# Performance work log

Measured on AMD Instinct MI355X. Metric: run time of the kernel, lower is better.

## Reference

```python
import jax, jax.numpy as jnp
import numpy as np

N = 10000      # nodes
E = 100000     # edges per direction
DIN = 128      # input feature dim (== hidden so layers stack)
H = 4          # attention heads
C = 128        # out channels per head (concat=False -> mean over heads)
ED = 16        # edge_attr dim
L = 2          # number of layers (len(hidden_sizes))
NEG_SLOPE = 0.2
EPS = 1e-5


def setup_inputs() -> dict:
    key = jax.random.key(0)
    ks = jax.random.split(key, 32)
    f32 = jnp.float32

    def nrm(k, shape, s=0.05):
        return jax.random.normal(k, shape, dtype=f32) * s

    inp = {}
    inp["x"] = nrm(ks[0], (N, DIN), 1.0)
    inp["fwd_edges_index"] = jax.random.randint(ks[1], (2, E), 0, N, dtype=jnp.int32)
    inp["bwd_edges_index"] = jax.random.randint(ks[2], (2, E), 0, N, dtype=jnp.int32)
    inp["edge_attr"] = nrm(ks[3], (E, ED), 1.0)
    # GATv2 params, stacked over layers; suffix _f = FWDGATLayer, _b = BWDGATLayer
    for i, sfx in enumerate(["f", "b"]):
        o = 4 + 7 * i
        inp[f"Wl_{sfx}"] = nrm(ks[o + 0], (L, DIN, H * C))   # lin_l (source x_j)
        inp[f"bl_{sfx}"] = jnp.zeros((L, H * C), f32)
        inp[f"Wr_{sfx}"] = nrm(ks[o + 1], (L, DIN, H * C))   # lin_r (target x_i)
        inp[f"br_{sfx}"] = jnp.zeros((L, H * C), f32)
        inp[f"We_{sfx}"] = nrm(ks[o + 2], (L, ED, H * C))    # lin_edge (no bias)
        inp[f"att_{sfx}"] = nrm(ks[o + 3], (L, H, C))        # attention vector a
        inp[f"bias_{sfx}"] = jnp.zeros((L, C), f32)          # final bias (concat=False)
    # Merge MLP: Linear(2C,C) -> ReLU -> Linear(C,C)
    inp["Wm1"] = nrm(ks[20], (L, 2 * C, C)); inp["bm1"] = jnp.zeros((L, C), f32)
    inp["Wm2"] = nrm(ks[21], (L, C, C));     inp["bm2"] = jnp.zeros((L, C), f32)
    # BatchNorm affine params (training-mode batch stats)
    inp["gamma"] = jnp.ones((L, C), f32)
    inp["beta"] = jnp.zeros((L, C), f32)
    return inp


def gatv2(x, src, dst, eattr, Wl, bl, Wr, br, We, att, bias):
    """PyG GATv2Conv, heads=H, concat=False (mean over heads), share_weights=False."""
    xl = (x @ Wl + bl).reshape(N, H, C)          # source-side transform (x_j)
    xr = (x @ Wr + br).reshape(N, H, C)          # target-side transform (x_i)
    ee = (eattr @ We).reshape(E, H, C)           # edge embedding
    z = jax.nn.leaky_relu(xl[src] + xr[dst] + ee, NEG_SLOPE)   # [E,H,C]
    logits = jnp.einsum('ehc,hc->eh', z, att)    # per-edge per-head scores
    # scatter-softmax over incoming edges of each target node
    amax = jax.lax.stop_gradient(jax.ops.segment_max(logits, dst, num_segments=N))
    amax = jnp.where(jnp.isfinite(amax), amax, 0.0)  # nodes with no in-edges
    ex = jnp.exp(logits - amax[dst])
    denom = jax.ops.segment_sum(ex, dst, num_segments=N)
    alpha = ex / denom[dst]                      # [E,H]
    msg = (xl[src] * alpha[:, :, None]).reshape(E, H * C)
    agg = jax.ops.segment_sum(msg, dst, num_segments=N).reshape(N, H, C)
    return agg.mean(axis=1) + bias               # concat=False -> head mean


def batch_norm(x, gamma, beta):
    mu = x.mean(axis=0)
    var = x.var(axis=0)  # biased var, as torch BN uses for normalization
    return gamma * (x - mu) * jax.lax.rsqrt(var + EPS) + beta


def reference(x, fwd_edges_index, bwd_edges_index, edge_attr,
              Wl_f, bl_f, Wr_f, br_f, We_f, att_f, bias_f,
              Wl_b, bl_b, Wr_b, br_b, We_b, att_b, bias_b,
              Wm1, bm1, Wm2, bm2, gamma, beta):
    fs, fd = fwd_edges_index[0], fwd_edges_index[1]
    bs, bd = bwd_edges_index[0], bwd_edges_index[1]
    h = x
    for l in range(L):
        f = gatv2(h, fs, fd, edge_attr, Wl_f[l], bl_f[l], Wr_f[l], br_f[l],
                  We_f[l], att_f[l], bias_f[l])
        b = gatv2(h, bs, bd, edge_attr, Wl_b[l], bl_b[l], Wr_b[l], br_b[l],
                  We_b[l], att_b[l], bias_b[l])
        m = jnp.concatenate([f, b], axis=1)                     # [N, 2C]
        m = jax.nn.relu(m @ Wm1[l] + bm1[l]) @ Wm2[l] + bm2[l]  # merge MLP
        h = jax.nn.relu(batch_norm(m, gamma[l], beta[l]))
    return h
```

## Files before the change

kernel.cpp:

```cpp
#include <hip/hip_runtime.h>

constexpr int N_  = 10000;
constexpr int E_  = 100000;
constexpr int MP_ = 10112;

typedef unsigned int u32;
typedef unsigned short u16;
typedef __attribute__((ext_vector_type(8))) _Float16 f16x8;
typedef __attribute__((ext_vector_type(4))) _Float16 f16x4;
typedef __attribute__((ext_vector_type(2))) _Float16 f16x2;
typedef __attribute__((ext_vector_type(4))) float f32x4;

__device__ __forceinline__ u16 f2h(float f) {
  _Float16 h = (_Float16)f;
  u16 r;
  __builtin_memcpy(&r, &h, 2);
  return r;
}
__device__ __forceinline__ void async16(const void* g, void* l) {
  __builtin_amdgcn_global_load_lds((const __attribute__((address_space(1))) u32*)g,
                                   (__attribute__((address_space(3))) u32*)l, 16, 0, 0);
}


__global__ void k_prep(const float* __restrict__ Wl_f, const float* __restrict__ Wr_f,
                       const float* __restrict__ Wl_b, const float* __restrict__ Wr_b,
                       const float* __restrict__ bl_f, const float* __restrict__ br_f,
                       const float* __restrict__ bl_b, const float* __restrict__ br_b,
                       const float* __restrict__ Wm1, const float* __restrict__ Wm2,
                       const float* __restrict__ We_f, const float* __restrict__ We_b,
                       u16* __restrict__ WCATh, float* __restrict__ BCAT,
                       u16* __restrict__ WM1h, u16* __restrict__ WM2h,
                       u16* __restrict__ WePh,
                       const float* __restrict__ x, u16* __restrict__ Xh,
                       const int* __restrict__ fdst, const int* __restrict__ bdst,
                       int* __restrict__ degf, int* __restrict__ degb) {
  int idx = blockIdx.x * 256 + threadIdx.x;
  if (idx < 2 * 2048 * 128) {
    int l = idx >> 18;
    int rem = idx & 262143;
    int j = rem >> 7, k = rem & 127;
    int grp = j >> 9, jj = j & 511;
    const float* W = grp == 0 ? Wl_f : grp == 1 ? Wr_f : grp == 2 ? Wl_b : Wr_b;
    WCATh[idx] = f2h(W[((size_t)(l * 128 + k)) * 512 + jj]);
  }
  if (idx < 2 * 2048) {
    int l = idx >> 11, j = idx & 2047;
    int grp = j >> 9, jj = j & 511;
    const float* bs = grp == 0 ? bl_f : grp == 1 ? br_f : grp == 2 ? bl_b : br_b;
    BCAT[idx] = bs[l * 512 + jj];
  }
  if (idx < 2 * 128 * 256) {
    int l = idx >> 15;
    int rem = idx & 32767;
    int n = rem >> 8, k = rem & 255;
    WM1h[idx] = f2h(Wm1[((size_t)(l * 256 + k)) * 128 + n]);
  }
  if (idx < 2 * 128 * 128) {
    int l = idx >> 14;
    int rem = idx & 16383;
    int n = rem >> 7, k = rem & 127;
    WM2h[idx] = f2h(Wm2[((size_t)(l * 128 + k)) * 128 + n]);
  }
  if (idx < 2 * 16384) {
    int dir = idx >> 14;
    int rem = idx & 16383;
    WePh[idx] = f2h((dir ? We_b : We_f)[rem]);
  }
  if (idx < MP_ * 32) {
    int row = idx >> 5;
    int c4 = (idx & 31) << 2;
    ushort4 o;
    if (row < N_) {
      float4 v = *reinterpret_cast<const float4*>(x + (size_t)row * 128 + c4);
      o.x = f2h(v.x); o.y = f2h(v.y); o.z = f2h(v.z); o.w = f2h(v.w);
    } else {
      o.x = o.y = o.z = o.w = 0;
    }
    *reinterpret_cast<ushort4*>(Xh + (size_t)row * 128 + c4) = o;
  }
  if (idx < E_) {
    atomicAdd(&degf[fdst[idx]], 1);
    atomicAdd(&degb[bdst[idx]], 1);
  }
}

__global__ void k_scan(const int* __restrict__ degf, const int* __restrict__ degb,
                       int* __restrict__ rpf, int* __restrict__ rpb,
                       int* __restrict__ permf, int* __restrict__ permb) {
  const int dir = blockIdx.x & 1;
  const int* deg = dir ? degb : degf;
  int t = threadIdx.x;
  __shared__ int lds[256];
  if (blockIdx.x < 2) {
    int* rp = dir ? rpb : rpf;
    const int CH = 40;
    int base = t * CH;
    int s = 0;
    for (int i = 0; i < CH; ++i) {
      int idx = base + i;
      if (idx < N_) s += deg[idx];
    }
    lds[t] = s;
    __syncthreads();
    for (int off = 1; off < 256; off <<= 1) {
      int v = (t >= off) ? lds[t - off] : 0;
      __syncthreads();
      lds[t] += v;
      __syncthreads();
    }
    int run = lds[t] - s;
    for (int i = 0; i < CH; ++i) {
      int idx = base + i;
      if (idx < N_) { rp[idx] = run; run += deg[idx]; }
    }
    if (t == 255) rp[N_] = lds[255];
  } else {
    int* perm = dir ? permb : permf;
    __shared__ int cnt[1024];
    __shared__ int off[1024];
    for (int i = t; i < 1024; i += 256) cnt[i] = 0;
    __syncthreads();
    for (int n = t; n < N_; n += 256) {
      int d = deg[n];
      if (d > 1023) d = 1023;
      atomicAdd(&cnt[d], 1);
    }
    __syncthreads();
    int s = 0;
#pragma unroll
    for (int i = 0; i < 4; ++i) s += cnt[1023 - (t * 4 + i)];
    lds[t] = s;
    __syncthreads();
    for (int o = 1; o < 256; o <<= 1) {
      int v = (t >= o) ? lds[t - o] : 0;
      __syncthreads();
      lds[t] += v;
      __syncthreads();
    }
    int run = lds[t] - s;
#pragma unroll
    for (int i = 0; i < 4; ++i) {
      int d = 1023 - (t * 4 + i);
      off[d] = run;
      run += cnt[d];
    }
    __syncthreads();
    for (int n = t; n < N_; n += 256) {
      int d = deg[n];
      if (d > 1023) d = 1023;
      int pos = atomicAdd(&off[d], 1);
      perm[pos] = n;
    }
  }
}

__global__ void k_scatter(const int* __restrict__ fwd, const int* __restrict__ bwd,
                          const int* __restrict__ rpf, const int* __restrict__ rpb,
                          int* __restrict__ curf, int* __restrict__ curb,
                          int* __restrict__ csf, int* __restrict__ csb,
                          u16* __restrict__ ePf, u16* __restrict__ ePb,
                          const float* __restrict__ eattr) {
  int e = blockIdx.x * 256 + threadIdx.x;
  if (e >= E_) return;
  const int dirb = blockIdx.y;
  const int* src = dirb ? bwd : fwd;
  const int* dst = (dirb ? bwd : fwd) + E_;
  const int* rp = dirb ? rpb : rpf;
  int* cur = dirb ? curb : curf;
  int* csrc = dirb ? csb : csf;
  u16* ePh = dirb ? ePb : ePf;
  int d = dst[e];
  int pos = rp[d] + atomicAdd(&cur[d], 1);
  csrc[pos] = src[e];
  const float4* s4 = reinterpret_cast<const float4*>(eattr + (size_t)e * 16);
  float4 a = s4[0], b = s4[1], c = s4[2], dd = s4[3];
  ushort4 o0, o1, o2, o3;
  o0.x = f2h(a.x); o0.y = f2h(a.y); o0.z = f2h(a.z); o0.w = f2h(a.w);
  o1.x = f2h(b.x); o1.y = f2h(b.y); o1.z = f2h(b.z); o1.w = f2h(b.w);
  o2.x = f2h(c.x); o2.y = f2h(c.y); o2.z = f2h(c.z); o2.w = f2h(c.w);
  o3.x = f2h(dd.x); o3.y = f2h(dd.y); o3.z = f2h(dd.z); o3.w = f2h(dd.w);
  ushort4* d4 = reinterpret_cast<ushort4*>(ePh + (size_t)pos * 16);
  d4[0] = o0; d4[1] = o1; d4[2] = o2; d4[3] = o3;
}


template <int K>
__global__ __launch_bounds__(256) void k_hgemm(const u16* __restrict__ A,
                                               const u16* __restrict__ Bt,
                                               const float* __restrict__ bias,
                                               u16* __restrict__ Cb, int M, int Ncols) {
  __shared__ __align__(16) u16 As[128 * 128];
  __shared__ __align__(16) u16 Bs[128 * 128];
  const int tid = threadIdx.x;
  const int lane = tid & 63, wave = tid >> 6;
  const int l16 = lane & 15, lq = lane >> 4;
  const int wm = wave & 1, wn = wave >> 1;
  const u16* Arow0 = A + (size_t)blockIdx.y * 128 * K;
  const u16* Brow0 = Bt + (size_t)blockIdx.x * 128 * K;

  f32x4 acc[4][4];
#pragma unroll
  for (int i = 0; i < 4; ++i)
#pragma unroll
    for (int j = 0; j < 4; ++j) acc[i][j] = (f32x4){0.f, 0.f, 0.f, 0.f};

  for (int kc = 0; kc < K; kc += 128) {
    if (kc) __syncthreads();
#pragma unroll
    for (int i = 0; i < 8; ++i) {
      int rg = i * 4 + wave;
      int r = rg * 4 + (lane >> 4);
      int cc = kc + (lane & 15) * 8;
      async16(Arow0 + (size_t)r * K + cc, (char*)As + rg * 1024);
      async16(Brow0 + (size_t)r * K + cc, (char*)Bs + rg * 1024);
    }
    __syncthreads();
    const u16* Ab = As + (wm * 64 + l16) * 128 + lq * 8;
    const u16* Bb = Bs + (wn * 64 + l16) * 128 + lq * 8;
#pragma unroll
    for (int ks = 0; ks < 4; ++ks) {
      f16x8 af[4], bfr[4];
#pragma unroll
      for (int j = 0; j < 4; ++j)
        af[j] = *reinterpret_cast<const f16x8*>(Ab + j * 16 * 128 + ks * 32);
#pragma unroll
      for (int i = 0; i < 4; ++i)
        bfr[i] = *reinterpret_cast<const f16x8*>(Bb + i * 16 * 128 + ks * 32);
#pragma unroll
      for (int i = 0; i < 4; ++i)
#pragma unroll
        for (int j = 0; j < 4; ++j)
          acc[i][j] = __builtin_amdgcn_mfma_f32_16x16x32_f16(bfr[i], af[j], acc[i][j], 0, 0, 0);
    }
  }

  const int node_base = blockIdx.y * 128 + wm * 64;
  const int col_base = blockIdx.x * 128 + wn * 64;
#pragma unroll
  for (int i = 0; i < 4; ++i) {
    int col0 = col_base + i * 16 + lq * 4;
    float4 bb = *reinterpret_cast<const float4*>(bias + col0);
#pragma unroll
    for (int j = 0; j < 4; ++j) {
      int node = node_base + j * 16 + l16;
      if (node < M) {
        ushort4 o;
        o.x = f2h(acc[i][j][0] + bb.x);
        o.y = f2h(acc[i][j][1] + bb.y);
        o.z = f2h(acc[i][j][2] + bb.z);
        o.w = f2h(acc[i][j][3] + bb.w);
        *reinterpret_cast<ushort4*>(Cb + (size_t)node * Ncols + col0) = o;
      }
    }
  }
}


__global__ __launch_bounds__(128, 4) void k_gat(
    const u16* __restrict__ XLXRh,
    const int* __restrict__ rpf, const int* __restrict__ csf, const u16* __restrict__ ePf,
    const int* __restrict__ rpb, const int* __restrict__ csb, const u16* __restrict__ ePb,
    const int* __restrict__ permf, const int* __restrict__ permb,
    const u16* __restrict__ WePh,
    const float* __restrict__ att_f, const float* __restrict__ att_b,
    const float* __restrict__ bias_f, const float* __restrict__ bias_b,
    u16* __restrict__ FBh, int layer) {
  const int dir = blockIdx.y;
  const int n = (dir ? permb : permf)[blockIdx.x];
  const int* rp = dir ? rpb : rpf;
  const int* cs = dir ? csb : csf;
  const u16* eP = dir ? ePb : ePf;
  const u16* WeP = WePh + dir * 16384 + layer * 8192;
  const float* att = (dir ? att_b : att_f) + layer * 512;
  const float* bias = (dir ? bias_b : bias_f) + layer * 128;
  const int t = threadIdx.x;
  const int ch = t << 2;
  const u16* XL = XLXRh + dir * 1024;
  const u16* XR = XL + 512;

  f32x4 a4 = *reinterpret_cast<const f32x4*>(att + ch);
  f16x4 xrh = *reinterpret_cast<const f16x4*>(XR + (size_t)n * 2048 + ch);
  f16x2 xr01 = {xrh.x, xrh.y}, xr23 = {xrh.z, xrh.w};
  f16x2 we01[16], we23[16];
#pragma unroll
  for (int k = 0; k < 16; ++k) {
    f16x4 w = *reinterpret_cast<const f16x4*>(WeP + k * 512 + ch);
    we01[k] = (f16x2){w.x, w.y};
    we23[k] = (f16x2){w.z, w.w};
  }

  auto pre = [&](f16x4 x, f16x8 eL, f16x8 eH) -> float {
    f16x2 z01 = (f16x2){x.x, x.y} + xr01;
    f16x2 z23 = (f16x2){x.z, x.w} + xr23;
#pragma unroll
    for (int k = 0; k < 16; ++k) {
      _Float16 sc = (k < 8) ? eL[k] : eH[k - 8];
      f16x2 c = {sc, sc};
      z01 = __builtin_elementwise_fma(c, we01[k], z01);
      z23 = __builtin_elementwise_fma(c, we23[k], z23);
    }
    const f16x2 hz = {(_Float16)0.f, (_Float16)0.f};
    const f16x2 hs = {(_Float16)0.2f, (_Float16)0.2f};
    f16x2 l01 = __builtin_elementwise_fma(hs, __builtin_elementwise_min(z01, hz),
                                          __builtin_elementwise_max(z01, hz));
    f16x2 l23 = __builtin_elementwise_fma(hs, __builtin_elementwise_min(z23, hz),
                                          __builtin_elementwise_max(z23, hz));
    return fmaf((float)l01.x, a4.x,
           fmaf((float)l01.y, a4.y,
           fmaf((float)l23.x, a4.z, (float)l23.y * a4.w)));
  };
  auto accum = [&](float ex, f16x4 x, f32x4& acc) {
    f32x4 xf = {(float)x.x, (float)x.y, (float)x.z, (float)x.w};
    acc = __builtin_elementwise_fma((f32x4){ex, ex, ex, ex}, xf, acc);
  };

  f32x4 acc = {0.f, 0.f, 0.f, 0.f};
  float denom = 0.f;
  const int s = rp[n], epos = rp[n + 1];
  int i = s;
  for (; i + 4 <= epos; i += 4) {
    int s0 = cs[i], s1 = cs[i + 1], s2 = cs[i + 2], s3 = cs[i + 3];
    f16x4 x0 = *reinterpret_cast<const f16x4*>(XL + (size_t)s0 * 2048 + ch);
    f16x4 x1 = *reinterpret_cast<const f16x4*>(XL + (size_t)s1 * 2048 + ch);
    f16x4 x2 = *reinterpret_cast<const f16x4*>(XL + (size_t)s2 * 2048 + ch);
    f16x4 x3 = *reinterpret_cast<const f16x4*>(XL + (size_t)s3 * 2048 + ch);
    f16x8 e0L = *reinterpret_cast<const f16x8*>(eP + (size_t)i * 16);
    f16x8 e0H = *reinterpret_cast<const f16x8*>(eP + (size_t)i * 16 + 8);
    f16x8 e1L = *reinterpret_cast<const f16x8*>(eP + (size_t)(i + 1) * 16);
    f16x8 e1H = *reinterpret_cast<const f16x8*>(eP + (size_t)(i + 1) * 16 + 8);
    f16x8 e2L = *reinterpret_cast<const f16x8*>(eP + (size_t)(i + 2) * 16);
    f16x8 e2H = *reinterpret_cast<const f16x8*>(eP + (size_t)(i + 2) * 16 + 8);
    f16x8 e3L = *reinterpret_cast<const f16x8*>(eP + (size_t)(i + 3) * 16);
    f16x8 e3H = *reinterpret_cast<const f16x8*>(eP + (size_t)(i + 3) * 16 + 8);
    float pA = pre(x0, e0L, e0H);
    float pB = pre(x1, e1L, e1H);
    float pC = pre(x2, e2L, e2H);
    float pD = pre(x3, e3L, e3H);
#pragma unroll
    for (int kk = 1; kk < 32; kk <<= 1) {
      pA += __shfl_xor(pA, kk, 32);
      pB += __shfl_xor(pB, kk, 32);
      pC += __shfl_xor(pC, kk, 32);
      pD += __shfl_xor(pD, kk, 32);
    }
    float ex0 = __expf(pA);
    float ex1 = __expf(pB);
    float ex2 = __expf(pC);
    float ex3 = __expf(pD);
    denom += (ex0 + ex1) + (ex2 + ex3);
    accum(ex0, x0, acc);
    accum(ex1, x1, acc);
    accum(ex2, x2, acc);
    accum(ex3, x3, acc);
  }
  for (; i < epos; ++i) {
    int s0 = cs[i];
    f16x4 x0 = *reinterpret_cast<const f16x4*>(XL + (size_t)s0 * 2048 + ch);
    f16x8 e0L = *reinterpret_cast<const f16x8*>(eP + (size_t)i * 16);
    f16x8 e0H = *reinterpret_cast<const f16x8*>(eP + (size_t)i * 16 + 8);
    float pA = pre(x0, e0L, e0H);
#pragma unroll
    for (int kk = 1; kk < 32; kk <<= 1) pA += __shfl_xor(pA, kk, 32);
    float ex0 = __expf(pA);
    denom += ex0;
    accum(ex0, x0, acc);
  }

  __shared__ __align__(16) float red[512];
  float inv = denom > 0.f ? 1.f / denom : 0.f;
  *reinterpret_cast<f32x4*>(&red[ch]) = acc * inv;
  __syncthreads();
  if (t < 32) {
    int c = t << 2;
    f32x4 r0 = *reinterpret_cast<const f32x4*>(&red[c]);
    f32x4 r1 = *reinterpret_cast<const f32x4*>(&red[c + 128]);
    f32x4 r2 = *reinterpret_cast<const f32x4*>(&red[c + 256]);
    f32x4 r3 = *reinterpret_cast<const f32x4*>(&red[c + 384]);
    f32x4 b4 = *reinterpret_cast<const f32x4*>(bias + c);
    f32x4 o = (r0 + r1 + r2 + r3) * 0.25f + b4;
    ushort4 oh;
    oh.x = f2h(o.x); oh.y = f2h(o.y); oh.z = f2h(o.z); oh.w = f2h(o.w);
    *reinterpret_cast<ushort4*>(FBh + (size_t)n * 256 + dir * 128 + c) = oh;
  }
}


__global__ __launch_bounds__(256) void k_mlp(const u16* __restrict__ FBh,
                                             const u16* __restrict__ W1,
                                             const float* __restrict__ b1,
                                             const u16* __restrict__ W2,
                                             const float* __restrict__ b2,
                                             float* __restrict__ M2,
                                             float* __restrict__ STATS) {
  __shared__ __align__(16) u16 As[128 * 128];
  __shared__ __align__(16) u16 Bs[64 * 128];
  __shared__ __align__(16) u16 M1s[64 * 128];
  __shared__ float ls[256];
  const int tid = threadIdx.x;
  const int lane = tid & 63, wave = tid >> 6;
  const int l16 = lane & 15, lq = lane >> 4;
  const int mb = blockIdx.x * 64;

  const int wr = wave & 1, wc = wave >> 1;
  f32x4 acc1[4][2];
#pragma unroll
  for (int i = 0; i < 4; ++i)
#pragma unroll
    for (int j = 0; j < 2; ++j) acc1[i][j] = (f32x4){0.f, 0.f, 0.f, 0.f};

  for (int kc = 0; kc < 256; kc += 128) {
    if (kc) __syncthreads();
#pragma unroll
    for (int tI = 0; tI < 8; ++tI) {
      int rg = tI * 4 + wave;
      int r = rg * 4 + (lane >> 4);
      async16(W1 + (size_t)r * 256 + kc + (lane & 15) * 8, (char*)As + rg * 1024);
    }
#pragma unroll
    for (int tI = 0; tI < 4; ++tI) {
      int rg = tI * 4 + wave;
      int r = rg * 4 + (lane >> 4);
      async16(FBh + (size_t)(mb + r) * 256 + kc + (lane & 15) * 8, (char*)Bs + rg * 1024);
    }
    __syncthreads();
#pragma unroll
    for (int ks = 0; ks < 4; ++ks) {
      f16x8 af[4], bfv[2];
#pragma unroll
      for (int i = 0; i < 4; ++i)
        af[i] = *reinterpret_cast<const f16x8*>(As + (wr * 64 + i * 16 + l16) * 128 + ks * 32 + lq * 8);
#pragma unroll
      for (int j = 0; j < 2; ++j)
        bfv[j] = *reinterpret_cast<const f16x8*>(Bs + (wc * 32 + j * 16 + l16) * 128 + ks * 32 + lq * 8);
#pragma unroll
      for (int i = 0; i < 4; ++i)
#pragma unroll
        for (int j = 0; j < 2; ++j)
          acc1[i][j] = __builtin_amdgcn_mfma_f32_16x16x32_f16(af[i], bfv[j], acc1[i][j], 0, 0, 0);
    }
  }
  ls[tid] = 0.f;
#pragma unroll
  for (int i = 0; i < 4; ++i) {
    float4 b1v = *reinterpret_cast<const float4*>(b1 + wr * 64 + i * 16 + lq * 4);
    float bb[4] = {b1v.x, b1v.y, b1v.z, b1v.w};
#pragma unroll
    for (int j = 0; j < 2; ++j) {
      int m = wc * 32 + j * 16 + l16;
      int k2 = wr * 64 + i * 16 + lq * 4;
      ushort4 o;
      o.x = f2h(fmaxf(acc1[i][j][0] + bb[0], 0.f));
      o.y = f2h(fmaxf(acc1[i][j][1] + bb[1], 0.f));
      o.z = f2h(fmaxf(acc1[i][j][2] + bb[2], 0.f));
      o.w = f2h(fmaxf(acc1[i][j][3] + bb[3], 0.f));
      *reinterpret_cast<ushort4*>(M1s + m * 128 + k2) = o;
    }
  }
  __syncthreads();
#pragma unroll
  for (int tI = 0; tI < 8; ++tI) {
    int rg = tI * 4 + wave;
    int r = rg * 4 + (lane >> 4);
    async16(W2 + (size_t)r * 128 + (lane & 15) * 8, (char*)As + rg * 1024);
  }
  __syncthreads();

  const int wr2 = wave & 1, wc2 = wave >> 1;
  f32x4 acc2[2][4];
#pragma unroll
  for (int i = 0; i < 2; ++i)
#pragma unroll
    for (int j = 0; j < 4; ++j) acc2[i][j] = (f32x4){0.f, 0.f, 0.f, 0.f};
#pragma unroll
  for (int ks = 0; ks < 4; ++ks) {
    f16x8 af2[2], bf2v[4];
#pragma unroll
    for (int i = 0; i < 2; ++i)
      af2[i] = *reinterpret_cast<const f16x8*>(M1s + (wr2 * 32 + i * 16 + l16) * 128 + ks * 32 + lq * 8);
#pragma unroll
    for (int j = 0; j < 4; ++j)
      bf2v[j] = *reinterpret_cast<const f16x8*>(As + (wc2 * 64 + j * 16 + l16) * 128 + ks * 32 + lq * 8);
#pragma unroll
    for (int i = 0; i < 2; ++i)
#pragma unroll
      for (int j = 0; j < 4; ++j)
        acc2[i][j] = __builtin_amdgcn_mfma_f32_16x16x32_f16(af2[i], bf2v[j], acc2[i][j], 0, 0, 0);
  }

  float s1[4] = {0.f, 0.f, 0.f, 0.f}, s2[4] = {0.f, 0.f, 0.f, 0.f};
  float b2j[4];
#pragma unroll
  for (int j = 0; j < 4; ++j) b2j[j] = b2[wc2 * 64 + j * 16 + l16];
#pragma unroll
  for (int i = 0; i < 2; ++i) {
#pragma unroll
    for (int r = 0; r < 4; ++r) {
      int m = mb + wr2 * 32 + i * 16 + lq * 4 + r;
      if (m < N_) {
#pragma unroll
        for (int j = 0; j < 4; ++j) {
          float v = acc2[i][j][r] + b2j[j];
          M2[(size_t)m * 128 + wc2 * 64 + j * 16 + l16] = v;
          s1[j] += v;
          s2[j] = fmaf(v, v, s2[j]);
        }
      }
    }
  }
#pragma unroll
  for (int j = 0; j < 4; ++j) {
    int c = wc2 * 64 + j * 16 + l16;
    atomicAdd(&ls[c], s1[j]);
    atomicAdd(&ls[128 + c], s2[j]);
  }
  __syncthreads();
  if (tid < 128) {
    atomicAdd(&STATS[tid], ls[tid]);
    atomicAdd(&STATS[128 + tid], ls[128 + tid]);
  }
}


__global__ void k_bn(const float* __restrict__ m2, const float* __restrict__ stats,
                     const float* __restrict__ gamma, const float* __restrict__ beta,
                     u16* __restrict__ houth, float* __restrict__ outf) {
  int idx = blockIdx.x * 256 + threadIdx.x;
  if (idx >= N_ * 32) return;
  int n = idx >> 5;
  int c = (idx & 31) << 2;
  float4 v = *reinterpret_cast<const float4*>(m2 + (size_t)n * 128 + c);
  const float invN = 1.f / (float)N_;
  float o[4];
  float vv[4] = {v.x, v.y, v.z, v.w};
#pragma unroll
  for (int q = 0; q < 4; ++q) {
    float mu = stats[c + q] * invN;
    float var = stats[128 + c + q] * invN - mu * mu;
    float rs = rsqrtf(var + 1e-5f);
    o[q] = fmaxf(gamma[c + q] * (vv[q] - mu) * rs + beta[c + q], 0.f);
  }
  ushort4 oh;
  oh.x = f2h(o[0]); oh.y = f2h(o[1]); oh.z = f2h(o[2]); oh.w = f2h(o[3]);
  *reinterpret_cast<ushort4*>(houth + (size_t)n * 128 + c) = oh;
  if (outf) {
    float4 of = make_float4(o[0], o[1], o[2], o[3]);
    *reinterpret_cast<float4*>(outf + (size_t)n * 128 + c) = of;
  }
}


extern "C" void kernel_launch(void* const* d_in, const int* in_sizes, int n_in,
                              void* d_out, int out_size, void* d_ws, size_t ws_size,
                              hipStream_t stream) {
  (void)in_sizes; (void)n_in; (void)out_size; (void)ws_size;
  const float* x      = (const float*)d_in[0];
  const int*   fwd    = (const int*)d_in[1];
  const int*   bwd    = (const int*)d_in[2];
  const float* eattr  = (const float*)d_in[3];
  const float* Wl_f   = (const float*)d_in[4];
  const float* bl_f   = (const float*)d_in[5];
  const float* Wr_f   = (const float*)d_in[6];
  const float* br_f   = (const float*)d_in[7];
  const float* We_f   = (const float*)d_in[8];
  const float* att_f  = (const float*)d_in[9];
  const float* bias_f = (const float*)d_in[10];
  const float* Wl_b   = (const float*)d_in[11];
  const float* bl_b   = (const float*)d_in[12];
  const float* Wr_b   = (const float*)d_in[13];
  const float* br_b   = (const float*)d_in[14];
  const float* We_b   = (const float*)d_in[15];
  const float* att_b  = (const float*)d_in[16];
  const float* bias_b = (const float*)d_in[17];
  const float* Wm1    = (const float*)d_in[18];
  const float* bm1    = (const float*)d_in[19];
  const float* Wm2    = (const float*)d_in[20];
  const float* bm2    = (const float*)d_in[21];
  const float* gamma  = (const float*)d_in[22];
  const float* beta   = (const float*)d_in[23];

  char* ws = (char*)d_ws;
  size_t off = 0;
  auto take = [&](size_t bytes) -> char* {
    char* p = ws + off;
    off += (bytes + 255) & ~(size_t)255;
    return p;
  };
  u16* WCATh = (u16*)take(2ull * 2048 * 128 * 2);
  float* BCAT = (float*)take(2ull * 2048 * 4);
  u16* WM1h = (u16*)take(2ull * 128 * 256 * 2);
  u16* WM2h = (u16*)take(2ull * 128 * 128 * 2);
  u16* WePh = (u16*)take(2ull * 16384 * 2);
  u16* Xh    = (u16*)take((size_t)MP_ * 128 * 2);
  u16* HBh   = (u16*)take((size_t)MP_ * 128 * 2);
  u16* XLXRh = (u16*)take((size_t)MP_ * 2048 * 2);
  u16* FBh   = (u16*)take((size_t)MP_ * 256 * 2);
  float* M2  = (float*)take((size_t)MP_ * 128 * 4);
  int* DEGS  = (int*)take(4ull * 40192);
  float* STATS = (float*)take(2ull * 256 * 4);
  int* degf = DEGS;
  int* degb = DEGS + (40192 / 4);
  int* curf = DEGS + 2 * (40192 / 4);
  int* curb = DEGS + 3 * (40192 / 4);
  int* rpf = (int*)take((N_ + 1) * 4);
  int* rpb = (int*)take((N_ + 1) * 4);
  int* csf = (int*)take((size_t)E_ * 4);
  int* csb = (int*)take((size_t)E_ * 4);
  int* permf = (int*)take((size_t)N_ * 4);
  int* permb = (int*)take((size_t)N_ * 4);
  u16* ePf = (u16*)take((size_t)E_ * 16 * 2 + 256);
  u16* ePb = (u16*)take((size_t)E_ * 16 * 2 + 256);

  hipMemsetAsync(DEGS, 0, 4ull * 40192 + 2ull * 256 * 4, stream);
  k_prep<<<2048, 256, 0, stream>>>(Wl_f, Wr_f, Wl_b, Wr_b, bl_f, br_f, bl_b, br_b,
                                   Wm1, Wm2, We_f, We_b, WCATh, BCAT, WM1h, WM2h, WePh,
                                   x, Xh, fwd + E_, bwd + E_, degf, degb);
  k_scan<<<4, 256, 0, stream>>>(degf, degb, rpf, rpb, permf, permb);
  k_scatter<<<dim3((E_ + 255) / 256, 2), 256, 0, stream>>>(
      fwd, bwd, rpf, rpb, curf, curb, csf, csb, ePf, ePb, eattr);

  for (int l = 0; l < 2; ++l) {
    const u16* hin = (l == 0) ? Xh : HBh;
    k_hgemm<128><<<dim3(16, MP_ / 128), 256, 0, stream>>>(
        hin, WCATh + (size_t)l * 2048 * 128, BCAT + l * 2048, XLXRh, N_, 2048);
    k_gat<<<dim3(N_, 2), 128, 0, stream>>>(XLXRh, rpf, csf, ePf, rpb, csb, ePb,
                                           permf, permb, WePh, att_f, att_b,
                                           bias_f, bias_b, FBh, l);
    k_mlp<<<MP_ / 64, 256, 0, stream>>>(FBh, WM1h + (size_t)l * 128 * 256, bm1 + l * 128,
                                        WM2h + (size_t)l * 128 * 128, bm2 + l * 128, M2,
                                        STATS + l * 256);
    k_bn<<<(N_ * 32 + 255) / 256, 256, 0, stream>>>(
        M2, STATS + l * 256, gamma + l * 128, beta + l * 128, HBh,
        (l == 1) ? (float*)d_out : nullptr);
  }
}
```

Baseline: 344.9 us.

## Fuse BatchNorm into merge-MLP kernel via grid-wide atomic barrier

Folds the BatchNorm+ReLU pass into the MLP kernel. Each block reduces its column stats with wave shuffles, adds them atomically to global stats, then waits at a spin-wait grid barrier built on a global counter before normalizing its tile straight from registers. This drops the fp32 M2 intermediate write and read and one kernel launch. The MFMA operands are swapped so each lane holds four consecutive columns for vectorized stores. The barrier relies on all 158 blocks being resident at once, which holds on this GPU but would deadlock if they could not all be co-scheduled.

```diff
diff --git a/kernel.cpp b/kernel.cpp
--- a/kernel.cpp
+++ b/kernel.cpp
@@ -3,6 +3,7 @@
 constexpr int N_  = 10000;
 constexpr int E_  = 100000;
 constexpr int MP_ = 10112;
+constexpr int NBLK_ = MP_ / 64;
 
 typedef unsigned int u32;
 typedef unsigned short u16;
@@ -391,12 +392,16 @@
                                              const float* __restrict__ b1,
                                              const u16* __restrict__ W2,
                                              const float* __restrict__ b2,
-                                             float* __restrict__ M2,
-                                             float* __restrict__ STATS) {
+                                             const float* __restrict__ gamma,
+                                             const float* __restrict__ beta,
+                                             float* __restrict__ STATS,
+                                             int* __restrict__ CTR,
+                                             u16* __restrict__ HBh,
+                                             float* __restrict__ outf) {
   __shared__ __align__(16) u16 As[128 * 128];
   __shared__ __align__(16) u16 Bs[64 * 128];
   __shared__ __align__(16) u16 M1s[64 * 128];
-  __shared__ float ls[256];
+  __shared__ float sA[128], sB[128];
   const int tid = threadIdx.x;
   const int lane = tid & 63, wave = tid >> 6;
   const int l16 = lane & 15, lq = lane >> 4;
@@ -440,7 +445,6 @@
           acc1[i][j] = __builtin_amdgcn_mfma_f32_16x16x32_f16(af[i], bfv[j], acc1[i][j], 0, 0, 0);
     }
   }
-  ls[tid] = 0.f;
 #pragma unroll
   for (int i = 0; i < 4; ++i) {
     float4 b1v = *reinterpret_cast<const float4*>(b1 + wr * 64 + i * 16 + lq * 4);
@@ -485,67 +489,96 @@
     for (int i = 0; i < 2; ++i)
 #pragma unroll
       for (int j = 0; j < 4; ++j)
-        acc2[i][j] = __builtin_amdgcn_mfma_f32_16x16x32_f16(af2[i], bf2v[j], acc2[i][j], 0, 0, 0);
-  }
-
-  float s1[4] = {0.f, 0.f, 0.f, 0.f}, s2[4] = {0.f, 0.f, 0.f, 0.f};
-  float b2j[4];
-#pragma unroll
-  for (int j = 0; j < 4; ++j) b2j[j] = b2[wc2 * 64 + j * 16 + l16];
+        acc2[i][j] = __builtin_amdgcn_mfma_f32_16x16x32_f16(bf2v[j], af2[i], acc2[i][j], 0, 0, 0);
+  }
+
+#pragma unroll
+  for (int j = 0; j < 4; ++j) {
+    float4 b2v = *reinterpret_cast<const float4*>(b2 + wc2 * 64 + j * 16 + lq * 4);
+    f32x4 bv = {b2v.x, b2v.y, b2v.z, b2v.w};
+#pragma unroll
+    for (int i = 0; i < 2; ++i) acc2[i][j] += bv;
+  }
+
+  f32x4 s1[4], s2[4];
+#pragma unroll
+  for (int j = 0; j < 4; ++j) { s1[j] = (f32x4){0.f,0.f,0.f,0.f}; s2[j] = (f32x4){0.f,0.f,0.f,0.f}; }
 #pragma unroll
   for (int i = 0; i < 2; ++i) {
-#pragma unroll
-    for (int r = 0; r < 4; ++r) {
-      int m = mb + wr2 * 32 + i * 16 + lq * 4 + r;
-      if (m < N_) {
-#pragma unroll
-        for (int j = 0; j < 4; ++j) {
-          float v = acc2[i][j][r] + b2j[j];
-          M2[(size_t)m * 128 + wc2 * 64 + j * 16 + l16] = v;
-          s1[j] += v;
-          s2[j] = fmaf(v, v, s2[j]);
+    int m = mb + wr2 * 32 + i * 16 + l16;
+    if (m < N_) {
+#pragma unroll
+      for (int j = 0; j < 4; ++j) {
+        s1[j] += acc2[i][j];
+        s2[j] += acc2[i][j] * acc2[i][j];
+      }
+    }
+  }
+#pragma unroll
+  for (int j = 0; j < 4; ++j) {
+#pragma unroll
+    for (int msk = 1; msk < 16; msk <<= 1) {
+#pragma unroll
+      for (int q = 0; q < 4; ++q) {
+        s1[j][q] += __shfl_xor(s1[j][q], msk, 16);
+        s2[j][q] += __shfl_xor(s2[j][q], msk, 16);
+      }
+    }
+  }
+  if (l16 == 0) {
+#pragma unroll
+    for (int j = 0; j < 4; ++j) {
+      int c0 = wc2 * 64 + j * 16 + lq * 4;
+#pragma unroll
+      for (int q = 0; q < 4; ++q) {
+        atomicAdd(&STATS[c0 + q], s1[j][q]);
+        atomicAdd(&STATS[128 + c0 + q], s2[j][q]);
+      }
+    }
+  }
+  __syncthreads();
+  if (tid == 0) {
+    __threadfence();
+    atomicAdd(CTR, 1);
+    while (__hip_atomic_load(CTR, __ATOMIC_ACQUIRE, __HIP_MEMORY_SCOPE_AGENT) < NBLK_) {
+      __builtin_amdgcn_s_sleep(16);
+    }
+  }
+  __syncthreads();
+
+  if (tid < 128) {
+    float sv1 = __hip_atomic_load(&STATS[tid], __ATOMIC_RELAXED, __HIP_MEMORY_SCOPE_AGENT);
+    float sv2 = __hip_atomic_load(&STATS[128 + tid], __ATOMIC_RELAXED, __HIP_MEMORY_SCOPE_AGENT);
+    const float invN = 1.f / (float)N_;
+    float mu = sv1 * invN;
+    float var = sv2 * invN - mu * mu;
+    float a = gamma[tid] * rsqrtf(var + 1e-5f);
+    sA[tid] = a;
+    sB[tid] = beta[tid] - mu * a;
+  }
+  __syncthreads();
+
+#pragma unroll
+  for (int i = 0; i < 2; ++i) {
+    int m = mb + wr2 * 32 + i * 16 + l16;
+    if (m < N_) {
+#pragma unroll
+      for (int j = 0; j < 4; ++j) {
+        int c0 = wc2 * 64 + j * 16 + lq * 4;
+        f32x4 av = *reinterpret_cast<const f32x4*>(&sA[c0]);
+        f32x4 bv = *reinterpret_cast<const f32x4*>(&sB[c0]);
+        f32x4 o = __builtin_elementwise_fma(av, acc2[i][j], bv);
+        const f32x4 zz = {0.f, 0.f, 0.f, 0.f};
+        o = __builtin_elementwise_max(o, zz);
+        ushort4 oh;
+        oh.x = f2h(o[0]); oh.y = f2h(o[1]); oh.z = f2h(o[2]); oh.w = f2h(o[3]);
+        *reinterpret_cast<ushort4*>(HBh + (size_t)m * 128 + c0) = oh;
+        if (outf) {
+          float4 of = make_float4(o[0], o[1], o[2], o[3]);
+          *reinterpret_cast<float4*>(outf + (size_t)m * 128 + c0) = of;
         }
       }
     }
-  }
-#pragma unroll
-  for (int j = 0; j < 4; ++j) {
-    int c = wc2 * 64 + j * 16 + l16;
-    atomicAdd(&ls[c], s1[j]);
-    atomicAdd(&ls[128 + c], s2[j]);
-  }
-  __syncthreads();
-  if (tid < 128) {
-    atomicAdd(&STATS[tid], ls[tid]);
-    atomicAdd(&STATS[128 + tid], ls[128 + tid]);
-  }
-}
-
-
-__global__ void k_bn(const float* __restrict__ m2, const float* __restrict__ stats,
-                     const float* __restrict__ gamma, const float* __restrict__ beta,
-                     u16* __restrict__ houth, float* __restrict__ outf) {
-  int idx = blockIdx.x * 256 + threadIdx.x;
-  if (idx >= N_ * 32) return;
-  int n = idx >> 5;
-  int c = (idx & 31) << 2;
-  float4 v = *reinterpret_cast<const float4*>(m2 + (size_t)n * 128 + c);
-  const float invN = 1.f / (float)N_;
-  float o[4];
-  float vv[4] = {v.x, v.y, v.z, v.w};
-#pragma unroll
-  for (int q = 0; q < 4; ++q) {
-    float mu = stats[c + q] * invN;
-    float var = stats[128 + c + q] * invN - mu * mu;
-    float rs = rsqrtf(var + 1e-5f);
-    o[q] = fmaxf(gamma[c + q] * (vv[q] - mu) * rs + beta[c + q], 0.f);
-  }
-  ushort4 oh;
-  oh.x = f2h(o[0]); oh.y = f2h(o[1]); oh.z = f2h(o[2]); oh.w = f2h(o[3]);
-  *reinterpret_cast<ushort4*>(houth + (size_t)n * 128 + c) = oh;
-  if (outf) {
-    float4 of = make_float4(o[0], o[1], o[2], o[3]);
-    *reinterpret_cast<float4*>(outf + (size_t)n * 128 + c) = of;
   }
 }
 
@@ -595,9 +628,9 @@
   u16* HBh   = (u16*)take((size_t)MP_ * 128 * 2);
   u16* XLXRh = (u16*)take((size_t)MP_ * 2048 * 2);
   u16* FBh   = (u16*)take((size_t)MP_ * 256 * 2);
-  float* M2  = (float*)take((size_t)MP_ * 128 * 4);
   int* DEGS  = (int*)take(4ull * 40192);
   float* STATS = (float*)take(2ull * 256 * 4);
+  int* CTR   = (int*)take(256);
   int* degf = DEGS;
   int* degb = DEGS + (40192 / 4);
   int* curf = DEGS + 2 * (40192 / 4);
@@ -611,7 +644,7 @@
   u16* ePf = (u16*)take((size_t)E_ * 16 * 2 + 256);
   u16* ePb = (u16*)take((size_t)E_ * 16 * 2 + 256);
 
-  hipMemsetAsync(DEGS, 0, 4ull * 40192 + 2ull * 256 * 4, stream);
+  hipMemsetAsync(DEGS, 0, 4ull * 40192 + 2ull * 256 * 4 + 256, stream);
   k_prep<<<2048, 256, 0, stream>>>(Wl_f, Wr_f, Wl_b, Wr_b, bl_f, br_f, bl_b, br_b,
                                    Wm1, Wm2, We_f, We_b, WCATh, BCAT, WM1h, WM2h, WePh,
                                    x, Xh, fwd + E_, bwd + E_, degf, degb);
@@ -626,11 +659,10 @@
     k_gat<<<dim3(N_, 2), 128, 0, stream>>>(XLXRh, rpf, csf, ePf, rpb, csb, ePb,
                                            permf, permb, WePh, att_f, att_b,
                                            bias_f, bias_b, FBh, l);
-    k_mlp<<<MP_ / 64, 256, 0, stream>>>(FBh, WM1h + (size_t)l * 128 * 256, bm1 + l * 128,
-                                        WM2h + (size_t)l * 128 * 128, bm2 + l * 128, M2,
-                                        STATS + l * 256);
-    k_bn<<<(N_ * 32 + 255) / 256, 256, 0, stream>>>(
-        M2, STATS + l * 256, gamma + l * 128, beta + l * 128, HBh,
-        (l == 1) ? (float*)d_out : nullptr);
-  }
-}
+    k_mlp<<<NBLK_, 256, 0, stream>>>(FBh, WM1h + (size_t)l * 128 * 256, bm1 + l * 128,
+                                     WM2h + (size_t)l * 128 * 128, bm2 + l * 128,
+                                     gamma + l * 128, beta + l * 128,
+                                     STATS + l * 256, CTR + l, HBh,
+                                     (l == 1) ? (float*)d_out : nullptr);
+  }
+}
```

After: 402.7 us. 16.7% more time.
